# Kernel optimization log

Measured on AMD Instinct MI355X. Metric: run time of the kernel, lower is better.

## Reference

```python
import jax, jax.numpy as jnp
import numpy as np

B, S, H = 4, 2048, 1024
I = 2816          # intermediate_size
E = 8             # num_experts
K = 2             # num_experts_per_token
AUX_COEF = 0.01


def setup_inputs() -> dict:
    key = jax.random.key(0)
    ks = jax.random.split(key, 5)
    scale = 0.02
    return {
        "hidden_states": jax.random.normal(ks[0], (B, S, H), dtype=jnp.float32),
        "gate_w": jax.random.normal(ks[1], (E, H), dtype=jnp.float32) * scale,   # router Linear weight [out=E, in=H]
        "Wg": jax.random.normal(ks[2], (E, I, H), dtype=jnp.float32) * scale,    # gate_proj weights
        "Wu": jax.random.normal(ks[3], (E, I, H), dtype=jnp.float32) * scale,    # up_proj weights
        "Wd": jax.random.normal(ks[4], (E, H, I), dtype=jnp.float32) * scale,    # down_proj weights
    }


def reference(hidden_states, gate_w, Wg, Wu, Wd):
    b, s, h = hidden_states.shape
    x = hidden_states.reshape(-1, h)                     # [T, H], T = b*s
    T = x.shape[0]

    # --- router (eval mode: no jitter noise) ---
    logits = jnp.einsum('th,eh->te', x, gate_w)          # [T, E]
    probs = jax.nn.softmax(logits, axis=-1)              # [T, E]
    w, idx = jax.lax.top_k(probs, K)                     # [T, K], [T, K]
    w = w / jnp.sum(w, axis=-1, keepdims=True)

    onehot = jax.nn.one_hot(idx, E, dtype=probs.dtype)   # [T, K, E]

    # --- auxiliary load-balancing loss (matches torch: mask summed over tokens, kept per-k) ---
    f_i = onehot.sum(axis=0) / T                         # [K, E]
    p_i = probs.mean(axis=0)                             # [E]
    aux_loss = E * jnp.sum(f_i * p_i) * AUX_COEF

    # per-token combine weight for each expert
    cw = jnp.einsum('tk,tke->te', w, onehot)             # [T, E]

    # --- expert SwiGLU FFNs, weighted combine (loop over fixed small E) ---
    out = jnp.zeros_like(x)
    for e in range(E):
        g = jax.nn.silu(x @ Wg[e].T)                     # [T, I]
        u = x @ Wu[e].T                                  # [T, I]
        out = out + cw[:, e:e + 1] * ((g * u) @ Wd[e].T) # [T, H]

    return out.reshape(b, s, h), aux_loss
```

## Files before the change

kernel.cpp:

```cpp
#include <hip/hip_runtime.h>

#define TT 8192
#define HD 1024
#define ID 2816
#define NE 8

typedef unsigned short u16;
typedef __attribute__((ext_vector_type(8))) __bf16 bf16x8;
typedef __attribute__((ext_vector_type(4))) float f32x4;

static constexpr int BM = 128;
static constexpr int BK = 64;
static constexpr int MAXSLOT = 17408;
static constexpr int MTILES  = 136;
static constexpr int NN1     = ID/BM;
static constexpr int G1      = MTILES*NN1;
static constexpr int G2      = MTILES*8*2;

struct Meta {
  u16   zeros[32];
  int   cnt[NE];
  float psum[NE];
  int   cursor[NE];
  int   seg[12];
};

static constexpr size_t OFF_XH    = 0;
static constexpr size_t OFF_WGH   = OFF_XH   + (size_t)TT*HD*2;
static constexpr size_t OFF_WUH   = OFF_WGH  + (size_t)NE*ID*HD*2;
static constexpr size_t OFF_WDH   = OFF_WUH  + (size_t)NE*ID*HD*2;
static constexpr size_t OFF_ACT   = OFF_WDH  + (size_t)NE*HD*ID*2;
static constexpr size_t OFF_PERM  = OFF_ACT  + (size_t)MAXSLOT*ID*2;
static constexpr size_t OFF_TID   = OFF_PERM + (size_t)MAXSLOT*4;
static constexpr size_t OFF_TSLOT = OFF_TID  + (size_t)TT*2*4;
static constexpr size_t OFF_TW    = OFF_TSLOT+ (size_t)TT*2*4;
static constexpr size_t OFF_META  = OFF_TW   + (size_t)TT*2*4;
static constexpr size_t WS_NEED   = OFF_META + sizeof(Meta);
static constexpr size_t OFF_Y     = OFF_WGH;

__device__ __forceinline__ u16 f2bf(float f) {
  unsigned u = __float_as_uint(f);
  u += 0x7FFFu + ((u >> 16) & 1u);
  return (u16)(u >> 16);
}
__device__ __forceinline__ float bf2f(u16 h) {
  return __uint_as_float(((unsigned)h) << 16);
}

__device__ __forceinline__ float dot4(float4 a, float4 b) {
  return a.x*b.x + a.y*b.y + a.z*b.z + a.w*b.w;
}

__device__ __forceinline__ void gll16(const void* g, void* l) {
  __builtin_amdgcn_global_load_lds(
      (const __attribute__((address_space(1))) void*)g,
      (__attribute__((address_space(3))) void*)l, 16, 0, 0);
}

__global__ void k_init(int* __restrict__ perm, Meta* __restrict__ meta) {
  int gid  = blockIdx.x*blockDim.x + threadIdx.x;
  int nthr = gridDim.x*blockDim.x;
  for (int i = gid; i < MAXSLOT; i += nthr) perm[i] = -1;
  if (gid < 32) meta->zeros[gid] = 0;
  if (gid < NE) { meta->cnt[gid]=0; meta->psum[gid]=0.f; meta->cursor[gid]=0; }
}

__global__ void k_router(const float* __restrict__ x, const float* __restrict__ gw,
                         int* __restrict__ tke, float* __restrict__ tkw,
                         u16* __restrict__ xh, Meta* __restrict__ meta) {
  __shared__ int   s_cnt[NE];
  __shared__ float s_ps[NE];
  int tid = threadIdx.x;
  if (tid < NE) { s_cnt[tid]=0; s_ps[tid]=0.f; }
  __syncthreads();
  int wv = tid>>6, ln = tid&63;
  for (int it = 0; it < 8; ++it) {
    int t = it*1024 + blockIdx.x*4 + wv;
    const float4* xp = (const float4*)(x + (size_t)t*HD + ln*16);
    float4 xv0=xp[0], xv1=xp[1], xv2=xp[2], xv3=xp[3];
    union { u16 h[8]; uint4 v; } r0, r1;
    r0.h[0]=f2bf(xv0.x); r0.h[1]=f2bf(xv0.y); r0.h[2]=f2bf(xv0.z); r0.h[3]=f2bf(xv0.w);
    r0.h[4]=f2bf(xv1.x); r0.h[5]=f2bf(xv1.y); r0.h[6]=f2bf(xv1.z); r0.h[7]=f2bf(xv1.w);
    r1.h[0]=f2bf(xv2.x); r1.h[1]=f2bf(xv2.y); r1.h[2]=f2bf(xv2.z); r1.h[3]=f2bf(xv2.w);
    r1.h[4]=f2bf(xv3.x); r1.h[5]=f2bf(xv3.y); r1.h[6]=f2bf(xv3.z); r1.h[7]=f2bf(xv3.w);
    uint4* xo = (uint4*)(xh + (size_t)t*HD + ln*16);
    xo[0] = r0.v; xo[1] = r1.v;
    float lg[NE];
    #pragma unroll
    for (int e=0;e<NE;++e) {
      const float4* gp = (const float4*)(gw + e*HD + ln*16);
      lg[e] = dot4(xv0,gp[0]) + dot4(xv1,gp[1]) + dot4(xv2,gp[2]) + dot4(xv3,gp[3]);
    }
    #pragma unroll
    for (int e=0;e<NE;++e) {
      #pragma unroll
      for (int off=32; off; off>>=1) lg[e] += __shfl_xor(lg[e], off);
    }
    if (ln == 0) {
      float mx = lg[0];
      #pragma unroll
      for (int e=1;e<NE;++e) mx = fmaxf(mx, lg[e]);
      float p[NE], s = 0.f;
      #pragma unroll
      for (int e=0;e<NE;++e) { p[e] = __expf(lg[e]-mx); s += p[e]; }
      float inv = 1.f/s;
      #pragma unroll
      for (int e=0;e<NE;++e) p[e] *= inv;
      int e1 = 0;
      #pragma unroll
      for (int e=1;e<NE;++e) if (p[e] > p[e1]) e1 = e;
      int e2 = (e1==0) ? 1 : 0;
      #pragma unroll
      for (int e=0;e<NE;++e) if (e!=e1 && p[e] > p[e2]) e2 = e;
      float ws2 = p[e1] + p[e2];
      tke[2*t]   = e1; tke[2*t+1] = e2;
      tkw[2*t]   = p[e1]/ws2; tkw[2*t+1] = p[e2]/ws2;
      atomicAdd(&s_cnt[e1], 1); atomicAdd(&s_cnt[e2], 1);
      #pragma unroll
      for (int e=0;e<NE;++e) atomicAdd(&s_ps[e], p[e]);
    }
  }
  __syncthreads();
  if (tid < NE) { atomicAdd(&meta->cnt[tid], s_cnt[tid]); atomicAdd(&meta->psum[tid], s_ps[tid]); }
}

__global__ void k_scan(Meta* __restrict__ meta, float* __restrict__ aux_out) {
  if (threadIdx.x == 0) {
    int s = 0;
    for (int e=0;e<NE;++e) { meta->seg[e] = s; s += ((meta->cnt[e]+BM-1)/BM)*BM; }
    meta->seg[NE] = s;
    float a = 0.f;
    for (int e=0;e<NE;++e)
      a += ((float)meta->cnt[e]/(float)TT) * (meta->psum[e]/(float)TT);
    aux_out[0] = (float)NE * 0.01f * a;
  }
}

__global__ void k_scatter(const int* __restrict__ tke,
                          Meta* __restrict__ meta, int* __restrict__ perm,
                          int* __restrict__ tslot) {
  int t = blockIdx.x*blockDim.x + threadIdx.x;
  if (t >= TT) return;
  for (int k=0;k<2;++k) {
    int e = tke[2*t+k];
    int pos = atomicAdd(&meta->cursor[e], 1);
    int slot = meta->seg[e] + pos;
    perm[slot]   = t;
    tslot[2*t+k] = slot;
  }
}

__global__ void k_cvt3(const float* __restrict__ s0, const float* __restrict__ s1,
                       const float* __restrict__ s2, u16* __restrict__ dst) {
  const long per = (long)NE*ID*HD/8;
  const long tot = 3*per;
  for (long idx = (long)blockIdx.x*blockDim.x + threadIdx.x; idx < tot;
       idx += (long)gridDim.x*blockDim.x) {
    const float* src = (idx < per) ? s0 : (idx < 2*per) ? s1 : s2;
    long local = (idx < per) ? idx : (idx < 2*per) ? idx-per : idx-2*per;
    const float4* s4 = (const float4*)(src + local*8);
    float4 a = s4[0], b = s4[1];
    union { u16 h[8]; uint4 v; } r;
    r.h[0]=f2bf(a.x); r.h[1]=f2bf(a.y); r.h[2]=f2bf(a.z); r.h[3]=f2bf(a.w);
    r.h[4]=f2bf(b.x); r.h[5]=f2bf(b.y); r.h[6]=f2bf(b.z); r.h[7]=f2bf(b.w);
    *(uint4*)(dst + idx*8) = r.v;
  }
}


__launch_bounds__(256, 2)
__global__ void k_gemm1(const u16* __restrict__ xh, const u16* __restrict__ wgh, const u16* __restrict__ wuh,
                        const int* __restrict__ perm, const Meta* __restrict__ meta, u16* __restrict__ act) {
  __shared__ u16 As[BM*BK], Gs[BM*BK], Us[BM*BK];
  int bid = blockIdx.x;
  int wg  = (bid&7)*(G1/8) + (bid>>3);
  int band = wg/176, r = wg%176;
  int mt = band*8 + (r&7);
  int m0 = mt*BM;
  int n0 = (r>>3)*BM;
  int total = meta->seg[NE];
  if (m0 >= total) return;
  int e = 0;
  #pragma unroll
  for (int i=1;i<NE;++i) if (m0 >= meta->seg[i]) e = i;
  int tid = threadIdx.x;
  int srow = tid>>3;
  int scol = ((tid&7) ^ (srow&7)) * 8;
  const u16* zp = meta->zeros;
  int tok[4];
  const u16* ap[4]; const u16* gp[4]; const u16* up[4];
  #pragma unroll
  for (int j=0;j<4;++j) {
    tok[j] = perm[m0 + srow + 32*j];
    ap[j]  = xh + (size_t)(tok[j]<0?0:tok[j])*HD + scol;
    size_t rr = (size_t)e*ID + n0 + srow + 32*j;
    gp[j]  = wgh + rr*HD + scol;
    up[j]  = wuh + rr*HD + scol;
  }
  u16* lA = As + tid*8; u16* lG = Gs + tid*8; u16* lU = Us + tid*8;
  int wv = tid>>6, ln = tid&63;
  int wr = (wv>>1)*64, wc = (wv&1)*64;
  int lr = ln&15, kq = ln>>4;
  int kx = lr&7;
  f32x4 accg[4][4] = {};
  f32x4 accu[4][4] = {};
  for (int k0 = 0; k0 < HD; k0 += BK) {
    #pragma unroll
    for (int j=0;j<4;++j) {
      gll16(tok[j]<0 ? (const void*)zp : (const void*)(ap[j]+k0), lA + j*2048);
      gll16(gp[j]+k0, lG + j*2048);
      gll16(up[j]+k0, lU + j*2048);
    }
    __syncthreads();
    #pragma unroll
    for (int h=0; h<2; ++h) {
      int koff = ((h*4 + kq) ^ kx) * 8;
      bf16x8 af[4], gf[4], uf[4];
      #pragma unroll
      for (int m=0;m<4;++m) af[m] = *(const bf16x8*)&As[(wr+m*16+lr)*BK + koff];
      #pragma unroll
      for (int n=0;n<4;++n) {
        gf[n] = *(const bf16x8*)&Gs[(wc+n*16+lr)*BK + koff];
        uf[n] = *(const bf16x8*)&Us[(wc+n*16+lr)*BK + koff];
      }
      #pragma unroll
      for (int m=0;m<4;++m)
        #pragma unroll
        for (int n=0;n<4;++n) {
          accg[m][n] = __builtin_amdgcn_mfma_f32_16x16x32_bf16(af[m], gf[n], accg[m][n], 0,0,0);
          accu[m][n] = __builtin_amdgcn_mfma_f32_16x16x32_bf16(af[m], uf[n], accu[m][n], 0,0,0);
        }
    }
    __syncthreads();
  }
  int rb = wr + (ln>>4)*4;
  int cb = n0 + wc + (ln&15);
  #pragma unroll
  for (int m=0;m<4;++m)
    #pragma unroll
    for (int j=0;j<4;++j) {
      size_t row = (size_t)(m0 + rb + m*16 + j);
      u16* ap2 = act + row*ID + cb;
      #pragma unroll
      for (int n=0;n<4;++n) {
        float g = accg[m][n][j], u = accu[m][n][j];
        float sv = g / (1.f + __expf(-g));
        ap2[n*16] = f2bf(sv*u);
      }
    }
}

__launch_bounds__(256, 3)
__global__ void k_gemm2(const u16* __restrict__ act, const u16* __restrict__ wdh,
                        const Meta* __restrict__ meta, u16* __restrict__ y) {
  __shared__ u16 As[BM*BK], Bs[BM*BK];
  int bid = blockIdx.x;
  int wg  = (bid&7)*(G2/8) + (bid>>3);
  int kh  = (wg >= G2/2) ? 1 : 0;
  int w2  = wg - kh*(G2/2);
  int band = w2>>6, r = w2&63;
  int mt = band*8 + (r&7);
  int m0 = mt*BM;
  int n0 = (r>>3)*BM;
  int total = meta->seg[NE];
  if (m0 >= total) return;
  int e = 0;
  #pragma unroll
  for (int i=1;i<NE;++i) if (m0 >= meta->seg[i]) e = i;
  int kbase = kh * (ID/2);
  u16* yh = y + (size_t)kh*MAXSLOT*HD;
  int tid = threadIdx.x;
  int srow = tid>>3;
  int scol = ((tid&7) ^ (srow&7)) * 8;
  const u16* ab = act + (size_t)(m0 + srow)*ID + kbase + scol;
  const u16* b0 = wdh + ((size_t)e*HD + n0 + srow)*ID + kbase + scol;
  u16* lA = As + tid*8; u16* lB = Bs + tid*8;
  int wv = tid>>6, ln = tid&63;
  int wr = (wv>>1)*64, wc = (wv&1)*64;
  int lr = ln&15, kq = ln>>4;
  int kx = lr&7;
  f32x4 acc[4][4] = {};
  for (int k0 = 0; k0 < ID/2; k0 += BK) {
    #pragma unroll
    for (int j=0;j<4;++j) {
      gll16(ab + (size_t)j*32*ID + k0, lA + j*2048);
      gll16(b0 + (size_t)j*32*ID + k0, lB + j*2048);
    }
    __syncthreads();
    #pragma unroll
    for (int h=0; h<2; ++h) {
      int koff = ((h*4 + kq) ^ kx) * 8;
      bf16x8 af[4], bf[4];
      #pragma unroll
      for (int m=0;m<4;++m) af[m] = *(const bf16x8*)&As[(wr+m*16+lr)*BK + koff];
      #pragma unroll
      for (int n=0;n<4;++n) bf[n] = *(const bf16x8*)&Bs[(wc+n*16+lr)*BK + koff];
      #pragma unroll
      for (int m=0;m<4;++m)
        #pragma unroll
        for (int n=0;n<4;++n)
          acc[m][n] = __builtin_amdgcn_mfma_f32_16x16x32_bf16(af[m], bf[n], acc[m][n], 0,0,0);
    }
    __syncthreads();
  }
  int rb = wr + (ln>>4)*4;
  int cb = n0 + wc + (ln&15);
  #pragma unroll
  for (int m=0;m<4;++m)
    #pragma unroll
    for (int j=0;j<4;++j) {
      u16* yp = yh + (size_t)(m0 + rb + m*16 + j)*HD + cb;
      #pragma unroll
      for (int n=0;n<4;++n) yp[n*16] = f2bf(acc[m][n][j]);
    }
}

__global__ void k_combine(const u16* __restrict__ y, const int* __restrict__ tslot,
                          const float* __restrict__ tkw, float* __restrict__ out) {
  int idx = blockIdx.x*blockDim.x + threadIdx.x;
  int t = idx >> 7;
  int c = (idx & 127) * 8;
  int s0 = tslot[2*t], s1 = tslot[2*t+1];
  float w0 = tkw[2*t], w1 = tkw[2*t+1];
  const size_t H2 = (size_t)MAXSLOT*HD;
  union { uint4 v; u16 h[8]; } a0, a1, b0, b1;
  a0.v = *(const uint4*)(y + (size_t)s0*HD + c);
  a1.v = *(const uint4*)(y + H2 + (size_t)s0*HD + c);
  b0.v = *(const uint4*)(y + (size_t)s1*HD + c);
  b1.v = *(const uint4*)(y + H2 + (size_t)s1*HD + c);
  float r[8];
  #pragma unroll
  for (int i=0;i<8;++i)
    r[i] = w0*(bf2f(a0.h[i]) + bf2f(a1.h[i])) + w1*(bf2f(b0.h[i]) + bf2f(b1.h[i]));
  float4 o0 = {r[0],r[1],r[2],r[3]}, o1 = {r[4],r[5],r[6],r[7]};
  float4* op = (float4*)(out + (size_t)t*HD + c);
  op[0] = o0; op[1] = o1;
}

extern "C" void kernel_launch(void* const* d_in, const int* in_sizes, int n_in,
                              void* d_out, int out_size, void* d_ws, size_t ws_size,
                              hipStream_t stream) {
  if (ws_size < WS_NEED) return;
  const float* x  = (const float*)d_in[0];
  const float* gw = (const float*)d_in[1];
  const float* Wg = (const float*)d_in[2];
  const float* Wu = (const float*)d_in[3];
  const float* Wd = (const float*)d_in[4];
  float* out = (float*)d_out;
  char* ws = (char*)d_ws;
  u16* xh   = (u16*)(ws + OFF_XH);
  u16* wgh  = (u16*)(ws + OFF_WGH);
  u16* wdh  = (u16*)(ws + OFF_WDH);
  u16* act  = (u16*)(ws + OFF_ACT);
  int* perm = (int*)(ws + OFF_PERM);
  int* tke  = (int*)(ws + OFF_TID);
  int* tslot= (int*)(ws + OFF_TSLOT);
  float* tkw= (float*)(ws + OFF_TW);
  Meta* meta= (Meta*)(ws + OFF_META);
  u16* y    = (u16*)(ws + OFF_Y);
  u16* wuh  = (u16*)(ws + OFF_WUH);

  k_init   <<<128, 256, 0, stream>>>(perm, meta);
  k_router <<<256, 256, 0, stream>>>(x, gw, tke, tkw, xh, meta);
  k_scan   <<<1, 64, 0, stream>>>(meta, out + (size_t)TT*HD);
  k_scatter<<<32, 256, 0, stream>>>(tke, meta, perm, tslot);
  k_cvt3   <<<4096, 256, 0, stream>>>(Wg, Wu, Wd, wgh);
  k_gemm1  <<<G1, 256, 0, stream>>>(xh, wgh, wuh, perm, meta, act);
  k_gemm2  <<<G2, 256, 0, stream>>>(act, wdh, meta, y);
  k_combine<<<TT*HD/8/256, 256, 0, stream>>>(y, tslot, tkw, out);
}
```

Baseline: 551.5 us.

## Fold weight fp32-to-bf16 conversion into router and gemm1 kernels

Measured after the change: 568.8 us. +3.1%, slower.

```diff
diff --git a/kernel.cpp b/kernel.cpp
--- a/kernel.cpp
+++ b/kernel.cpp
@@ -16,6 +16,9 @@
 static constexpr int NN1     = ID/BM;
 static constexpr int G1      = MTILES*NN1;
 static constexpr int G2      = MTILES*8*2;
+static constexpr int RTR_BLK = 256;
+static constexpr int RTR_CVT = 1024;
+static constexpr int G1_CVT  = 512;
 
 struct Meta {
   u16   zeros[32];
@@ -57,6 +60,15 @@
       (__attribute__((address_space(3))) void*)l, 16, 0, 0);
 }
 
+__device__ __forceinline__ void cvt8(const float* __restrict__ src, u16* __restrict__ dst) {
+  const float4* s4 = (const float4*)src;
+  float4 a = s4[0], b = s4[1];
+  union { u16 h[8]; uint4 v; } r;
+  r.h[0]=f2bf(a.x); r.h[1]=f2bf(a.y); r.h[2]=f2bf(a.z); r.h[3]=f2bf(a.w);
+  r.h[4]=f2bf(b.x); r.h[5]=f2bf(b.y); r.h[6]=f2bf(b.z); r.h[7]=f2bf(b.w);
+  *(uint4*)dst = r.v;
+}
+
 __global__ void k_init(int* __restrict__ perm, Meta* __restrict__ meta) {
   int gid  = blockIdx.x*blockDim.x + threadIdx.x;
   int nthr = gridDim.x*blockDim.x;
@@ -67,7 +79,18 @@
 
 __global__ void k_router(const float* __restrict__ x, const float* __restrict__ gw,
                          int* __restrict__ tke, float* __restrict__ tkw,
-                         u16* __restrict__ xh, Meta* __restrict__ meta) {
+                         u16* __restrict__ xh, Meta* __restrict__ meta,
+                         const float* __restrict__ Wg, const float* __restrict__ Wu,
+                         u16* __restrict__ wgh) {
+  if (blockIdx.x >= RTR_BLK) {
+    const long per = (long)NE*ID*HD/8;
+    long base = (long)(blockIdx.x - RTR_BLK)*256 + threadIdx.x;
+    for (long idx = base; idx < 2*per; idx += (long)RTR_CVT*256) {
+      const float* src = (idx < per) ? (Wg + idx*8) : (Wu + (idx-per)*8);
+      cvt8(src, wgh + idx*8);
+    }
+    return;
+  }
   __shared__ int   s_cnt[NE];
   __shared__ float s_ps[NE];
   int tid = threadIdx.x;
@@ -150,29 +173,20 @@
   }
 }
 
-__global__ void k_cvt3(const float* __restrict__ s0, const float* __restrict__ s1,
-                       const float* __restrict__ s2, u16* __restrict__ dst) {
-  const long per = (long)NE*ID*HD/8;
-  const long tot = 3*per;
-  for (long idx = (long)blockIdx.x*blockDim.x + threadIdx.x; idx < tot;
-       idx += (long)gridDim.x*blockDim.x) {
-    const float* src = (idx < per) ? s0 : (idx < 2*per) ? s1 : s2;
-    long local = (idx < per) ? idx : (idx < 2*per) ? idx-per : idx-2*per;
-    const float4* s4 = (const float4*)(src + local*8);
-    float4 a = s4[0], b = s4[1];
-    union { u16 h[8]; uint4 v; } r;
-    r.h[0]=f2bf(a.x); r.h[1]=f2bf(a.y); r.h[2]=f2bf(a.z); r.h[3]=f2bf(a.w);
-    r.h[4]=f2bf(b.x); r.h[5]=f2bf(b.y); r.h[6]=f2bf(b.z); r.h[7]=f2bf(b.w);
-    *(uint4*)(dst + idx*8) = r.v;
-  }
-}
-
 
 __launch_bounds__(256, 2)
 __global__ void k_gemm1(const u16* __restrict__ xh, const u16* __restrict__ wgh, const u16* __restrict__ wuh,
-                        const int* __restrict__ perm, const Meta* __restrict__ meta, u16* __restrict__ act) {
+                        const int* __restrict__ perm, const Meta* __restrict__ meta, u16* __restrict__ act,
+                        const float* __restrict__ Wd, u16* __restrict__ wdh) {
   __shared__ u16 As[BM*BK], Gs[BM*BK], Us[BM*BK];
   int bid = blockIdx.x;
+  if (bid >= G1) {
+    const long per = (long)NE*ID*HD/8;
+    long base = (long)(bid - G1)*256 + threadIdx.x;
+    for (long idx = base; idx < per; idx += (long)G1_CVT*256)
+      cvt8(Wd + idx*8, wdh + idx*8);
+    return;
+  }
   int wg  = (bid&7)*(G1/8) + (bid>>3);
   int band = wg/176, r = wg%176;
   int mt = band*8 + (r&7);
@@ -361,11 +375,10 @@
   u16* wuh  = (u16*)(ws + OFF_WUH);
 
   k_init   <<<128, 256, 0, stream>>>(perm, meta);
-  k_router <<<256, 256, 0, stream>>>(x, gw, tke, tkw, xh, meta);
+  k_router <<<RTR_BLK + RTR_CVT, 256, 0, stream>>>(x, gw, tke, tkw, xh, meta, Wg, Wu, wgh);
   k_scan   <<<1, 64, 0, stream>>>(meta, out + (size_t)TT*HD);
   k_scatter<<<32, 256, 0, stream>>>(tke, meta, perm, tslot);
-  k_cvt3   <<<4096, 256, 0, stream>>>(Wg, Wu, Wd, wgh);
-  k_gemm1  <<<G1, 256, 0, stream>>>(xh, wgh, wuh, perm, meta, act);
+  k_gemm1  <<<G1 + G1_CVT, 256, 0, stream>>>(xh, wgh, wuh, perm, meta, act, Wd, wdh);
   k_gemm2  <<<G2, 256, 0, stream>>>(act, wdh, meta, y);
   k_combine<<<TT*HD/8/256, 256, 0, stream>>>(y, tslot, tkw, out);
 }
```
